# Optimization experiments

Measured on AMD Instinct MI355X. Metric: run time of the kernel, lower is better.

## Reference

```python
import jax, jax.numpy as jnp
import numpy as np

K = 7      # unfold_size
P = 3      # unfold_size // 2
EPS = 1e-5 # batchnorm eps


def _conv1x1(x, w, b=None):
    # x: (B,C,H,W), w: (O,C)
    y = jnp.einsum('bchw,oc->bohw', x, w)
    if b is not None:
        y = y + b[None, :, None, None]
    return y


def _bn(x, g, b, m, v):
    # eval-mode batchnorm over channel axis 1
    inv = jax.lax.rsqrt(v + EPS)
    return (x - m[None, :, None, None]) * (g * inv)[None, :, None, None] + b[None, :, None, None]


def setup_inputs() -> dict:
    key = jax.random.key(0)
    ks = jax.random.split(key, 18)
    B, C, MID, H, W = 8, 256, 64, 64, 64
    rn = lambda k, s, sc=1.0: jax.random.normal(k, s, dtype=jnp.float32) * sc
    ru = lambda k, s: jax.random.uniform(k, s, dtype=jnp.float32)
    return {
        'x':     rn(ks[0], (B, C, H, W)),
        'w_red': rn(ks[1], (MID, C), 0.05),
        'w_c':   rn(ks[2], (3, MID, MID, 3, 3), 0.05),
        'b_c':   rn(ks[3], (3, MID), 0.05),
        'bn_g':  ru(ks[4], (3, MID)) * 0.5 + 0.75,
        'bn_b':  rn(ks[5], (3, MID), 0.05),
        'bn_m':  rn(ks[6], (3, MID), 0.05),
        'bn_v':  ru(ks[7], (3, MID)) + 0.5,
        'w_out': rn(ks[8], (C, MID), 0.05),
        'b_out': rn(ks[9], (C,), 0.05),
        'bno_g': ru(ks[10], (C,)) * 0.5 + 0.75,
        'bno_b': rn(ks[11], (C,), 0.05),
        'bno_m': rn(ks[12], (C,), 0.05),
        'bno_v': ru(ks[13], (C,)) + 0.5,
        'w_f1':  rn(ks[14], (C, C), 0.05),
        'b_f1':  rn(ks[15], (C,), 0.05),
        'w_f2':  rn(ks[16], (C, C), 0.05),
        'b_f2':  rn(ks[17], (C,), 0.05),
    }


def reference(x, w_red, w_c, b_c, bn_g, bn_b, bn_m, bn_v,
              w_out, b_out, bno_g, bno_b, bno_m, bno_v,
              w_f1, b_f1, w_f2, b_f2):
    B, C, H, W = x.shape
    MID = w_red.shape[0]

    # channel reduction + L2 normalize over channels (F.normalize, eps=1e-12)
    q = _conv1x1(x, w_red)                                   # (B,MID,H,W)
    q = q / jnp.maximum(jnp.linalg.norm(q, axis=1, keepdims=True), 1e-12)

    # SelfCorrelationComputation: unfold KxK with padding P, multiply by center, clamp >= 0
    qp = jnp.pad(q, ((0, 0), (0, 0), (P, P), (P, P)))
    pats = jnp.stack([qp[:, :, i:i + H, j:j + W]
                      for i in range(K) for j in range(K)], axis=2)  # (B,MID,K*K,H,W)
    ss = jnp.maximum(pats * q[:, :, None], 0.0)              # (B,MID,49,H,W)

    # SelfSimilarityEncoder: conv3d with (1,ksize,ksize) kernel == batched 2D conv over (u,v)
    ss = ss.transpose(0, 3, 4, 1, 2).reshape(B * H * W, MID, K, K)  # (B*HW,MID,K,K)
    dn = ('NCHW', 'OIHW', 'NCHW')
    y = ss
    for i in range(3):  # unfold_size // 2 blocks; 7 -> 5 -> 3 -> 1
        y = jax.lax.conv_general_dilated(y, w_c[i], (1, 1), 'VALID', dimension_numbers=dn)
        y = y + b_c[i][None, :, None, None]
        y = jnp.maximum(_bn(y, bn_g[i], bn_b[i], bn_m[i], bn_v[i]), 0.0)
    y = y.mean(axis=(-1, -2)).reshape(B, H, W, MID).transpose(0, 3, 1, 2)  # (B,MID,H,W)
    feat = _bn(_conv1x1(y, w_out, b_out), bno_g, bno_b, bno_m, bno_v)      # (B,C,H,W)

    # residual + FFN (1x1 conv -> relu -> 1x1 conv)
    out = x + feat
    out = _conv1x1(jnp.maximum(_conv1x1(out, w_f1, b_f1), 0.0), w_f2, b_f2)
    return out
```

## Files before the change

### kernel.cpp

```cpp
#include <hip/hip_runtime.h>
#include <stdint.h>


typedef __attribute__((ext_vector_type(8))) __bf16 bf16x8;
typedef __attribute__((ext_vector_type(4))) float f32x4;

__device__ __forceinline__ ushort f2bf(float f) {
  uint32_t u = __builtin_bit_cast(uint32_t, f);
  u += 0x7fffu + ((u >> 16) & 1u);
  return (ushort)(u >> 16);
}
__device__ __forceinline__ float bfu(ushort h) {
  return __builtin_bit_cast(float, ((uint32_t)h) << 16);
}
__device__ __forceinline__ f32x4 mfma16(bf16x8 a, bf16x8 b, f32x4 c) {
  return __builtin_amdgcn_mfma_f32_16x16x32_bf16(a, b, c, 0, 0, 0);
}

union BV8 { uint4 v; ushort u[8]; };

#define OFF_WRT 0u
#define OFF_WCB 65536u
#define OFF_SHC 286720u
#define OFF_WOB 287488u
#define OFF_SHO 320256u
#define OFF_WF1 321280u
#define OFF_WF2 452352u
#define OFF_QN  583424u
#define OFF_Y   4777728u

__global__ __launch_bounds__(256) void k_prep(
    const float* __restrict__ w_red, const float* __restrict__ w_c, const float* __restrict__ b_c,
    const float* __restrict__ bn_g, const float* __restrict__ bn_b, const float* __restrict__ bn_m,
    const float* __restrict__ bn_v, const float* __restrict__ w_out, const float* __restrict__ b_out,
    const float* __restrict__ bno_g, const float* __restrict__ bno_b, const float* __restrict__ bno_m,
    const float* __restrict__ bno_v, const float* __restrict__ w_f1, const float* __restrict__ w_f2,
    float* __restrict__ w_red_t, ushort* __restrict__ wc_b, float* __restrict__ shift_c,
    ushort* __restrict__ w_out_b, float* __restrict__ shift_o,
    ushort* __restrict__ w_f1_b, ushort* __restrict__ w_f2_b)
{
  int i = blockIdx.x * 256 + threadIdx.x;
  if (i < 16384) {
    int c = i >> 6, m = i & 63;
    w_red_t[i] = w_red[m * 256 + c];
    return;
  }
  i -= 16384;
  if (i < 110592) {
    int c = i & 63, o = (i >> 6) & 63, st = i >> 12;
    int tap = st % 9, s = st / 9;
    float sc = bn_g[s * 64 + o] * rsqrtf(bn_v[s * 64 + o] + 1e-5f);
    wc_b[i] = f2bf(w_c[((s * 64 + o) * 64 + c) * 9 + tap] * sc);
    return;
  }
  i -= 110592;
  if (i < 192) {
    int s = i >> 6, o = i & 63;
    float sc = bn_g[s * 64 + o] * rsqrtf(bn_v[s * 64 + o] + 1e-5f);
    shift_c[i] = (b_c[i] - bn_m[i]) * sc + bn_b[i];
    return;
  }
  i -= 192;
  if (i < 16384) {
    int o = i >> 6;
    float sc = bno_g[o] * rsqrtf(bno_v[o] + 1e-5f);
    w_out_b[i] = f2bf(w_out[i] * sc);
    return;
  }
  i -= 16384;
  if (i < 256) {
    float sc = bno_g[i] * rsqrtf(bno_v[i] + 1e-5f);
    shift_o[i] = (b_out[i] - bno_m[i]) * sc + bno_b[i];
    return;
  }
  i -= 256;
  if (i < 65536) { w_f1_b[i] = f2bf(w_f1[i]); return; }
  i -= 65536;
  if (i < 65536) { w_f2_b[i] = f2bf(w_f2[i]); return; }
}

__global__ __launch_bounds__(256) void k_qnorm(
    const float* __restrict__ x, const float* __restrict__ w_red_t, ushort* __restrict__ qn)
{
  __shared__ float xs[64 * 64];
  __shared__ float wls[64 * 64];
  __shared__ float part[64 * 16];
  __shared__ float sinv[64];

  const int tid = threadIdx.x;
  const int pix0 = blockIdx.x * 64;
  const int b = pix0 >> 12;
  const int hw0 = pix0 & 4095;
  const int pxq = tid & 15, mq = tid >> 4;
  const int lr = tid >> 2, lseg = tid & 3;

  float acc[4][4] = {};

  for (int c0 = 0; c0 < 256; c0 += 64) {
    const float4* xg = (const float4*)(x + (size_t)(b * 256 + c0 + lr) * 4096 + hw0 + lseg * 16);
    float4* xd = (float4*)(xs + lr * 64 + lseg * 16);
    const float4* wg = (const float4*)(w_red_t + (c0 + lr) * 64 + lseg * 16);
    float4* wd = (float4*)(wls + lr * 64 + lseg * 16);
#pragma unroll
    for (int j = 0; j < 4; ++j) xd[j] = xg[j];
#pragma unroll
    for (int j = 0; j < 4; ++j) wd[j] = wg[j];
    __syncthreads();
    for (int c = 0; c < 64; ++c) {
      float4 xv = *(const float4*)(xs + c * 64 + pxq * 4);
      float4 wv = *(const float4*)(wls + c * 64 + mq * 4);
      float xa[4] = {xv.x, xv.y, xv.z, xv.w};
      float wa[4] = {wv.x, wv.y, wv.z, wv.w};
#pragma unroll
      for (int mi = 0; mi < 4; ++mi)
#pragma unroll
        for (int pi = 0; pi < 4; ++pi)
          acc[mi][pi] = fmaf(wa[mi], xa[pi], acc[mi][pi]);
    }
    __syncthreads();
  }

#pragma unroll
  for (int pi = 0; pi < 4; ++pi) {
    float s = 0.f;
#pragma unroll
    for (int mi = 0; mi < 4; ++mi) s += acc[mi][pi] * acc[mi][pi];
    part[(pxq * 4 + pi) * 16 + mq] = s;
  }
  __syncthreads();
  if (tid < 64) {
    float s = 0.f;
#pragma unroll
    for (int k = 0; k < 16; ++k) s += part[tid * 16 + k];
    sinv[tid] = 1.0f / fmaxf(sqrtf(s), 1e-12f);
  }
  __syncthreads();
#pragma unroll
  for (int pi = 0; pi < 4; ++pi) {
    const int px = pxq * 4 + pi;
    const float inv = sinv[px];
    ushort4 v;
    v.x = f2bf(acc[0][pi] * inv);
    v.y = f2bf(acc[1][pi] * inv);
    v.z = f2bf(acc[2][pi] * inv);
    v.w = f2bf(acc[3][pi] * inv);
    *(ushort4*)(qn + (size_t)(pix0 + px) * 64 + mq * 4) = v;
  }
}

#define ENC_RING 7168
#define ENC_O1   14336
#define SMEM_ENC 79872

__device__ __forceinline__ void store_act(ushort* buf, int pos, int n, int q, int o0,
                                          f32x4 acc, float4 sh) {
  ushort4 v;
  v.x = f2bf(fmaxf(acc[0] + sh.x, 0.0f));
  v.y = f2bf(fmaxf(acc[1] + sh.y, 0.0f));
  v.z = f2bf(fmaxf(acc[2] + sh.z, 0.0f));
  v.w = f2bf(fmaxf(acc[3] + sh.w, 0.0f));
  const int chunk = (o0 >> 3) + (q >> 1);
  *(ushort4*)(buf + (pos * 16 + n) * 64 + ((chunk ^ (n & 7)) * 8) + (q & 1) * 4) = v;
}

__device__ __forceinline__ void build_row(
    ushort* dstslot, const ushort* __restrict__ qn,
    int b, int tr, int tc, int ir, int tid)
{
  for (int u0 = tid; u0 < 896; u0 += 256) {
    const int ch = u0 & 7, px = (u0 >> 3) & 15, dv = u0 >> 7;
    const int ph = tr + (px >> 2), pw = tc + (px & 3);
    const int nh = ph + ir - 3, nw = pw + dv - 3;
    uint4 ov4;
    if ((unsigned)nh < 64u && (unsigned)nw < 64u) {
      BV8 cv; cv.v = *(const uint4*)(qn + (size_t)((b << 12) + ph * 64 + pw) * 64 + ch * 8);
      BV8 nv; nv.v = *(const uint4*)(qn + (size_t)((b << 12) + nh * 64 + nw) * 64 + ch * 8);
      BV8 ov;
#pragma unroll
      for (int j = 0; j < 8; ++j)
        ov.u[j] = f2bf(fmaxf(bfu(nv.u[j]) * bfu(cv.u[j]), 0.0f));
      ov4 = ov.v;
    } else {
      ov4 = make_uint4(0u, 0u, 0u, 0u);
    }
    *(uint4*)(dstslot + (dv * 16 + px) * 64 + ((ch ^ (px & 7)) * 8)) = ov4;
  }
}

__global__ __launch_bounds__(256, 2) void k_encoder(
    const ushort* __restrict__ qn, const ushort* __restrict__ wc_b,
    const float* __restrict__ shift_c, ushort* __restrict__ yout)
{
  extern __shared__ char smem[];
  ushort* enc = (ushort*)smem;
  ushort* o1 = enc + ENC_O1;

  const int tid = threadIdx.x;
  const int b = blockIdx.z;
  const int tr = blockIdx.y * 4;
  const int tc = blockIdx.x * 4;

  const int lane = tid & 63, wv = tid >> 6;
  const int n = lane & 15, q = lane >> 4;
  const int o0 = wv * 16;
  const int sw = n & 7;
  const int rowoff = n * 64;
  const int c0 = ((0 + q) ^ sw) * 8;
  const int c1 = ((4 + q) ^ sw) * 8;

  bf16x8 af[18];
#pragma unroll
  for (int t = 0; t < 9; ++t) {
    af[t * 2]     = *(const bf16x8*)(wc_b + (t * 64 + o0 + n) * 64 + q * 8);
    af[t * 2 + 1] = *(const bf16x8*)(wc_b + (t * 64 + o0 + n) * 64 + 32 + q * 8);
  }

  const f32x4 zero = {0.f, 0.f, 0.f, 0.f};
  f32x4 acc[5][5];
#pragma unroll
  for (int u = 0; u < 5; ++u)
#pragma unroll
    for (int v = 0; v < 5; ++v) acc[u][v] = zero;

  build_row(enc, qn, b, tr, tc, 0, tid);
  __syncthreads();

#pragma unroll
  for (int ir = 0; ir < 7; ++ir) {
    if (ir < 6)
      build_row(enc + ((ir + 1) & 1) * ENC_RING, qn, b, tr, tc, ir + 1, tid);
    {
      const ushort* rowb = enc + (ir & 1) * ENC_RING + rowoff;
      bf16x8 rf0[7], rf1[7];
#pragma unroll
      for (int j = 0; j < 7; ++j) {
        rf0[j] = *(const bf16x8*)(rowb + j * 1024 + c0);
        rf1[j] = *(const bf16x8*)(rowb + j * 1024 + c1);
      }
#pragma unroll
      for (int u = 0; u < 5; ++u) {
        const int du = ir - u;
        if (du >= 0 && du < 3) {
#pragma unroll
          for (int dv = 0; dv < 3; ++dv)
#pragma unroll
            for (int v = 0; v < 5; ++v) {
              acc[u][v] = mfma16(af[(du * 3 + dv) * 2],     rf0[v + dv], acc[u][v]);
              acc[u][v] = mfma16(af[(du * 3 + dv) * 2 + 1], rf1[v + dv], acc[u][v]);
            }
        }
      }
    }
    if (ir < 6) __syncthreads();
  }

  {
    const float4 sh = *(const float4*)(shift_c + o0 + q * 4);
#pragma unroll
    for (int u = 0; u < 5; ++u)
#pragma unroll
      for (int v = 0; v < 5; ++v)
        store_act(o1, u * 5 + v, n, q, o0, acc[u][v], sh);
  }
  __syncthreads();

  {
#pragma unroll
    for (int t = 0; t < 9; ++t) {
      af[t * 2]     = *(const bf16x8*)(wc_b + 9 * 4096 + (t * 64 + o0 + n) * 64 + q * 8);
      af[t * 2 + 1] = *(const bf16x8*)(wc_b + 9 * 4096 + (t * 64 + o0 + n) * 64 + 32 + q * 8);
    }
    f32x4 acc2[3][3];
#pragma unroll
    for (int u = 0; u < 3; ++u)
#pragma unroll
      for (int v = 0; v < 3; ++v) acc2[u][v] = zero;

#pragma unroll
    for (int ir = 0; ir < 5; ++ir) {
      const ushort* rowb = o1 + ir * 5 * 1024 + rowoff;
      bf16x8 rf0[5], rf1[5];
#pragma unroll
      for (int j = 0; j < 5; ++j) {
        rf0[j] = *(const bf16x8*)(rowb + j * 1024 + c0);
        rf1[j] = *(const bf16x8*)(rowb + j * 1024 + c1);
      }
#pragma unroll
      for (int u = 0; u < 3; ++u) {
        const int du = ir - u;
        if (du >= 0 && du < 3) {
#pragma unroll
          for (int dv = 0; dv < 3; ++dv)
#pragma unroll
            for (int v = 0; v < 3; ++v) {
              acc2[u][v] = mfma16(af[(du * 3 + dv) * 2],     rf0[v + dv], acc2[u][v]);
              acc2[u][v] = mfma16(af[(du * 3 + dv) * 2 + 1], rf1[v + dv], acc2[u][v]);
            }
        }
      }
    }
    const float4 sh = *(const float4*)(shift_c + 64 + o0 + q * 4);
#pragma unroll
    for (int u = 0; u < 3; ++u)
#pragma unroll
      for (int v = 0; v < 3; ++v)
        store_act(enc, u * 3 + v, n, q, o0, acc2[u][v], sh);
  }
  __syncthreads();

  {
#pragma unroll
    for (int t = 0; t < 9; ++t) {
      af[t * 2]     = *(const bf16x8*)(wc_b + 18 * 4096 + (t * 64 + o0 + n) * 64 + q * 8);
      af[t * 2 + 1] = *(const bf16x8*)(wc_b + 18 * 4096 + (t * 64 + o0 + n) * 64 + 32 + q * 8);
    }
    f32x4 a0 = zero, a1 = zero;
#pragma unroll
    for (int tap = 0; tap < 9; ++tap) {
      const ushort* rA = enc + tap * 1024 + rowoff;
      a0 = mfma16(af[tap * 2],     *(const bf16x8*)(rA + c0), a0);
      a1 = mfma16(af[tap * 2 + 1], *(const bf16x8*)(rA + c1), a1);
    }
    f32x4 acc3 = a0 + a1;
    const float4 sh = *(const float4*)(shift_c + 128 + o0 + q * 4);
    ushort4 v;
    v.x = f2bf(fmaxf(acc3[0] + sh.x, 0.0f));
    v.y = f2bf(fmaxf(acc3[1] + sh.y, 0.0f));
    v.z = f2bf(fmaxf(acc3[2] + sh.z, 0.0f));
    v.w = f2bf(fmaxf(acc3[3] + sh.w, 0.0f));
    const int ph = tr + (n >> 2), pw = tc + (n & 3);
    *(ushort4*)(yout + (size_t)((b << 12) + ph * 64 + pw) * 64 + o0 + q * 4) = v;
  }
}

#define SMEM_OUT (2 * 64 * 256 * 2)

__global__ __launch_bounds__(256) void k_out(
    const ushort* __restrict__ y, const float* __restrict__ x,
    const ushort* __restrict__ w_out_b, const float* __restrict__ shift_o,
    const ushort* __restrict__ w_f1_b, const float* __restrict__ b_f1,
    const ushort* __restrict__ w_f2_b, const float* __restrict__ b_f2,
    float* __restrict__ out)
{
  extern __shared__ char smem[];
  ushort* rls = (ushort*)smem;
  ushort* hls = (ushort*)(smem + 64 * 256 * 2);

  const int tid = threadIdx.x, lane = tid & 63, wv = tid >> 6;
  const int n = lane & 15, q = lane >> 4;
  const int pix0 = blockIdx.x * 64;
  const int b = pix0 >> 12, hw0 = pix0 & 4095;
  const int sw = n & 7;
  const f32x4 zero = {0.f, 0.f, 0.f, 0.f};

  {
    bf16x8 wa[8];
#pragma unroll
    for (int mt = 0; mt < 4; ++mt) {
      const int ob = wv * 64 + mt * 16;
      wa[mt * 2]     = *(const bf16x8*)(w_out_b + (ob + n) * 64 + q * 8);
      wa[mt * 2 + 1] = *(const bf16x8*)(w_out_b + (ob + n) * 64 + 32 + q * 8);
    }
    for (int nt = 0; nt < 4; ++nt) {
      const int px0 = nt * 16;
      const bf16x8 yb0 = *(const bf16x8*)(y + (size_t)(pix0 + px0 + n) * 64 + q * 8);
      const bf16x8 yb1 = *(const bf16x8*)(y + (size_t)(pix0 + px0 + n) * 64 + 32 + q * 8);
#pragma unroll
      for (int mt = 0; mt < 4; ++mt) {
        const int ob = wv * 64 + mt * 16;
        f32x4 acc = zero;
        acc = mfma16(wa[mt * 2], yb0, acc);
        acc = mfma16(wa[mt * 2 + 1], yb1, acc);
        const float4 sh = *(const float4*)(shift_o + ob + q * 4);
        const float sha[4] = {sh.x, sh.y, sh.z, sh.w};
        ushort tmp[4];
#pragma unroll
        for (int r = 0; r < 4; ++r) {
          const int o = ob + q * 4 + r;
          const float xv = x[(size_t)(b * 256 + o) * 4096 + hw0 + px0 + n];
          tmp[r] = f2bf(xv + acc[r] + sha[r]);
        }
        ushort4 v; v.x = tmp[0]; v.y = tmp[1]; v.z = tmp[2]; v.w = tmp[3];
        const int chunk = (ob >> 3) + (q >> 1);
        *(ushort4*)(rls + (px0 + n) * 256 + ((chunk ^ sw) * 8) + (q & 1) * 4) = v;
      }
    }
  }
  __syncthreads();

  {
    bf16x8 wf[32];
#pragma unroll
    for (int mt = 0; mt < 4; ++mt)
#pragma unroll
      for (int kc = 0; kc < 8; ++kc)
        wf[mt * 8 + kc] = *(const bf16x8*)(w_f1_b + (size_t)(wv * 64 + mt * 16 + n) * 256 + kc * 32 + q * 8);
    for (int nt = 0; nt < 4; ++nt) {
      const int px0 = nt * 16;
      bf16x8 rb[8];
#pragma unroll
      for (int kc = 0; kc < 8; ++kc)
        rb[kc] = *(const bf16x8*)(rls + (px0 + n) * 256 + (((kc * 4 + q) ^ sw) * 8));
#pragma unroll
      for (int mt = 0; mt < 4; ++mt) {
        const int ob = wv * 64 + mt * 16;
        f32x4 a0 = zero, a1 = zero;
#pragma unroll
        for (int kc = 0; kc < 8; kc += 2) {
          a0 = mfma16(wf[mt * 8 + kc], rb[kc], a0);
          a1 = mfma16(wf[mt * 8 + kc + 1], rb[kc + 1], a1);
        }
        f32x4 acc = a0 + a1;
        const float4 bb = *(const float4*)(b_f1 + ob + q * 4);
        const float bba[4] = {bb.x, bb.y, bb.z, bb.w};
        ushort tmp[4];
#pragma unroll
        for (int r = 0; r < 4; ++r) tmp[r] = f2bf(fmaxf(acc[r] + bba[r], 0.0f));
        ushort4 v; v.x = tmp[0]; v.y = tmp[1]; v.z = tmp[2]; v.w = tmp[3];
        const int chunk = (ob >> 3) + (q >> 1);
        *(ushort4*)(hls + (px0 + n) * 256 + ((chunk ^ sw) * 8) + (q & 1) * 4) = v;
      }
    }
  }
  __syncthreads();

  {
    bf16x8 wf[32];
#pragma unroll
    for (int mt = 0; mt < 4; ++mt)
#pragma unroll
      for (int kc = 0; kc < 8; ++kc)
        wf[mt * 8 + kc] = *(const bf16x8*)(w_f2_b + (size_t)(wv * 64 + mt * 16 + n) * 256 + kc * 32 + q * 8);
    for (int nt = 0; nt < 4; ++nt) {
      const int px0 = nt * 16;
      bf16x8 rb[8];
#pragma unroll
      for (int kc = 0; kc < 8; ++kc)
        rb[kc] = *(const bf16x8*)(hls + (px0 + n) * 256 + (((kc * 4 + q) ^ sw) * 8));
#pragma unroll
      for (int mt = 0; mt < 4; ++mt) {
        const int ob = wv * 64 + mt * 16;
        f32x4 a0 = zero, a1 = zero;
#pragma unroll
        for (int kc = 0; kc < 8; kc += 2) {
          a0 = mfma16(wf[mt * 8 + kc], rb[kc], a0);
          a1 = mfma16(wf[mt * 8 + kc + 1], rb[kc + 1], a1);
        }
        f32x4 acc = a0 + a1;
        const float4 bb = *(const float4*)(b_f2 + ob + q * 4);
        const float bba[4] = {bb.x, bb.y, bb.z, bb.w};
#pragma unroll
        for (int r = 0; r < 4; ++r) {
          const int o = ob + q * 4 + r;
          out[(size_t)(b * 256 + o) * 4096 + hw0 + px0 + n] = acc[r] + bba[r];
        }
      }
    }
  }
}

extern "C" void kernel_launch(void* const* d_in, const int* in_sizes, int n_in,
                              void* d_out, int out_size, void* d_ws, size_t ws_size,
                              hipStream_t stream) {
  const float* x     = (const float*)d_in[0];
  const float* w_red = (const float*)d_in[1];
  const float* w_c   = (const float*)d_in[2];
  const float* b_c   = (const float*)d_in[3];
  const float* bn_g  = (const float*)d_in[4];
  const float* bn_b  = (const float*)d_in[5];
  const float* bn_m  = (const float*)d_in[6];
  const float* bn_v  = (const float*)d_in[7];
  const float* w_out = (const float*)d_in[8];
  const float* b_out = (const float*)d_in[9];
  const float* bno_g = (const float*)d_in[10];
  const float* bno_b = (const float*)d_in[11];
  const float* bno_m = (const float*)d_in[12];
  const float* bno_v = (const float*)d_in[13];
  const float* w_f1  = (const float*)d_in[14];
  const float* b_f1  = (const float*)d_in[15];
  const float* w_f2  = (const float*)d_in[16];
  const float* b_f2  = (const float*)d_in[17];

  char* ws = (char*)d_ws;
  float*  w_red_t = (float*)(ws + OFF_WRT);
  ushort* wc_b    = (ushort*)(ws + OFF_WCB);
  float*  shift_c = (float*)(ws + OFF_SHC);
  ushort* w_out_b = (ushort*)(ws + OFF_WOB);
  float*  shift_o = (float*)(ws + OFF_SHO);
  ushort* w_f1_b  = (ushort*)(ws + OFF_WF1);
  ushort* w_f2_b  = (ushort*)(ws + OFF_WF2);
  ushort* qnb     = (ushort*)(ws + OFF_QN);
  ushort* yb      = (ushort*)(ws + OFF_Y);

  k_prep<<<1074, 256, 0, stream>>>(w_red, w_c, b_c, bn_g, bn_b, bn_m, bn_v,
                                   w_out, b_out, bno_g, bno_b, bno_m, bno_v,
                                   w_f1, w_f2,
                                   w_red_t, wc_b, shift_c, w_out_b, shift_o, w_f1_b, w_f2_b);
  k_qnorm<<<512, 256, 0, stream>>>(x, w_red_t, qnb);
  k_encoder<<<dim3(16, 16, 8), 256, SMEM_ENC, stream>>>(qnb, wc_b, shift_c, yb);
  k_out<<<512, 256, SMEM_OUT, stream>>>(yb, x, w_out_b, shift_o, w_f1_b, b_f1, w_f2_b, b_f2,
                                        (float*)d_out);
}
```

Baseline: 273.6 us.

## Prefetch encoder neighbour rows into registers to overlap global loads with MFMA

The per-row patch build in the encoder is split into an issue phase, which loads neighbour vectors into registers, and a write phase, which multiplies, clamps and stores them to LDS. The center vectors and index math are hoisted out of the row loop. Loads for row ir+2 are issued after the MFMA work for row ir, so global latency can hide behind compute. The bf16 conversion also switches to the compiler's native __bf16 cast. This adds registers in a kernel already holding large accumulator and weight arrays, which risks spills or lower occupancy.

```diff
diff --git a/kernel.cpp b/kernel.cpp
--- a/kernel.cpp
+++ b/kernel.cpp
@@ -6,9 +6,8 @@
 typedef __attribute__((ext_vector_type(4))) float f32x4;
 
 __device__ __forceinline__ ushort f2bf(float f) {
-  uint32_t u = __builtin_bit_cast(uint32_t, f);
-  u += 0x7fffu + ((u >> 16) & 1u);
-  return (ushort)(u >> 16);
+  __bf16 h = (__bf16)f;
+  return __builtin_bit_cast(ushort, h);
 }
 __device__ __forceinline__ float bfu(ushort h) {
   return __builtin_bit_cast(float, ((uint32_t)h) << 16);
@@ -163,30 +162,6 @@
   *(ushort4*)(buf + (pos * 16 + n) * 64 + ((chunk ^ (n & 7)) * 8) + (q & 1) * 4) = v;
 }
 
-__device__ __forceinline__ void build_row(
-    ushort* dstslot, const ushort* __restrict__ qn,
-    int b, int tr, int tc, int ir, int tid)
-{
-  for (int u0 = tid; u0 < 896; u0 += 256) {
-    const int ch = u0 & 7, px = (u0 >> 3) & 15, dv = u0 >> 7;
-    const int ph = tr + (px >> 2), pw = tc + (px & 3);
-    const int nh = ph + ir - 3, nw = pw + dv - 3;
-    uint4 ov4;
-    if ((unsigned)nh < 64u && (unsigned)nw < 64u) {
-      BV8 cv; cv.v = *(const uint4*)(qn + (size_t)((b << 12) + ph * 64 + pw) * 64 + ch * 8);
-      BV8 nv; nv.v = *(const uint4*)(qn + (size_t)((b << 12) + nh * 64 + nw) * 64 + ch * 8);
-      BV8 ov;
-#pragma unroll
-      for (int j = 0; j < 8; ++j)
-        ov.u[j] = f2bf(fmaxf(bfu(nv.u[j]) * bfu(cv.u[j]), 0.0f));
-      ov4 = ov.v;
-    } else {
-      ov4 = make_uint4(0u, 0u, 0u, 0u);
-    }
-    *(uint4*)(dstslot + (dv * 16 + px) * 64 + ((ch ^ (px & 7)) * 8)) = ov4;
-  }
-}
-
 __global__ __launch_bounds__(256, 2) void k_encoder(
     const ushort* __restrict__ qn, const ushort* __restrict__ wc_b,
     const float* __restrict__ shift_c, ushort* __restrict__ yout)
@@ -208,6 +183,51 @@
   const int c0 = ((0 + q) ^ sw) * 8;
   const int c1 = ((4 + q) ^ sw) * 8;
 
+  int chk[4], nwk[4], dstk[4], phk[4];
+  bool actk[4], nwok[4];
+  uint4 cenR[4], nbrR[4];
+#pragma unroll
+  for (int k = 0; k < 4; ++k) {
+    const int u0 = tid + k * 256;
+    actk[k] = (u0 < 896);
+    const int ch = u0 & 7, px = (u0 >> 3) & 15, dv = (u0 >> 7) & 7;
+    chk[k] = ch;
+    const int ph = tr + (px >> 2), pw = tc + (px & 3);
+    phk[k] = ph;
+    nwk[k] = pw + dv - 3;
+    nwok[k] = actk[k] && ((unsigned)nwk[k] < 64u);
+    dstk[k] = (dv * 16 + px) * 64 + ((ch ^ (px & 7)) * 8);
+    cenR[k] = make_uint4(0u, 0u, 0u, 0u);
+    if (actk[k])
+      cenR[k] = *(const uint4*)(qn + (size_t)((b << 12) + ph * 64 + pw) * 64 + ch * 8);
+  }
+
+#define ENC_ISSUE(r)                                                              \
+  {                                                                               \
+    _Pragma("unroll")                                                             \
+    for (int k = 0; k < 4; ++k) {                                                 \
+      const int nh = phk[k] + (r) - 3;                                            \
+      if (nwok[k] && (unsigned)nh < 64u)                                          \
+        nbrR[k] = *(const uint4*)(qn + (size_t)((b << 12) + nh * 64 + nwk[k]) * 64 \
+                                  + chk[k] * 8);                                  \
+      else                                                                        \
+        nbrR[k] = make_uint4(0u, 0u, 0u, 0u);                                     \
+    }                                                                             \
+  }
+#define ENC_WRITE(slot)                                                           \
+  {                                                                               \
+    _Pragma("unroll")                                                             \
+    for (int k = 0; k < 4; ++k) {                                                 \
+      if (actk[k]) {                                                              \
+        BV8 cv, nv, ov; cv.v = cenR[k]; nv.v = nbrR[k];                           \
+        _Pragma("unroll")                                                         \
+        for (int j = 0; j < 8; ++j)                                               \
+          ov.u[j] = f2bf(fmaxf(bfu(nv.u[j]) * bfu(cv.u[j]), 0.0f));               \
+        *(uint4*)((slot) + dstk[k]) = ov.v;                                       \
+      }                                                                           \
+    }                                                                             \
+  }
+
   bf16x8 af[18];
 #pragma unroll
   for (int t = 0; t < 9; ++t) {
@@ -222,13 +242,13 @@
 #pragma unroll
     for (int v = 0; v < 5; ++v) acc[u][v] = zero;
 
-  build_row(enc, qn, b, tr, tc, 0, tid);
+  ENC_ISSUE(0);
+  ENC_WRITE(enc);
+  ENC_ISSUE(1);
   __syncthreads();
 
 #pragma unroll
   for (int ir = 0; ir < 7; ++ir) {
-    if (ir < 6)
-      build_row(enc + ((ir + 1) & 1) * ENC_RING, qn, b, tr, tc, ir + 1, tid);
     {
       const ushort* rowb = enc + (ir & 1) * ENC_RING + rowoff;
       bf16x8 rf0[7], rf1[7];
@@ -251,7 +271,11 @@
         }
       }
     }
-    if (ir < 6) __syncthreads();
+    if (ir < 6) {
+      ENC_WRITE(enc + ((ir + 1) & 1) * ENC_RING);
+      if (ir < 5) ENC_ISSUE(ir + 2);
+      __syncthreads();
+    }
   }
 
   {
```

Result: slower. 355.6 us (+30.0%).
